# Kernel optimization log

Hardware: AMD Instinct MI355X
Metric: run time of the kernel (lower is better)

## Reference

```python
import jax, jax.numpy as jnp
import numpy as np

H = W = 192
C = 256
MAX_FEATURES = 2048
NUM_UP = 4  # num_upsampling scaling steps: pos -> pos*2 + 0.5 each step

# HandcraftedLocalizationModule filters (D2-Net)
DI  = [[0., -0.5, 0.], [0., 0., 0.], [0., 0.5, 0.]]
DJ  = [[0., 0., 0.], [-0.5, 0., 0.5], [0., 0., 0.]]
DII = [[0., 1., 0.], [0., -2., 0.], [0., 1., 0.]]
DJJ = [[0., 0., 0.], [1., -2., 1.], [0., 0., 0.]]
DIJ = [[0.25, 0., -0.25], [0., 0., 0.], [-0.25, 0., 0.25]]


def _conv3(x, k):
    # x: [H,W]; 3x3 cross-correlation, padding 1 (matches F.conv2d)
    k = jnp.asarray(k, x.dtype)
    return jax.lax.conv_general_dilated(x[None, None], k[None, None],
                                        window_strides=(1, 1),
                                        padding=[(1, 1), (1, 1)])[0, 0]


def _process_scale(feat, score):
    # feat: [C,H,W] dense descriptors, score: [H,W] attention/detection map
    Hm, Wm = score.shape
    # --- NMS: 3x3 maxpool, keep only local maxima (x[lmax != x] = 0) ---
    lmax = jax.lax.reduce_window(score, -jnp.inf, jax.lax.max,
                                 (3, 3), (1, 1), [(1, 1), (1, 1)])
    det = jnp.where(lmax == score, score, 0.0)
    valid = det != 0.0  # torch.nonzero equivalent (fixed-shape mask)
    # --- handcrafted localization (2x2 Newton step on the raw score map) ---
    di, dj = _conv3(score, DI), _conv3(score, DJ)
    dii, djj, dij = _conv3(score, DII), _conv3(score, DJJ), _conv3(score, DIJ)
    dd = dii * djj - dij * dij
    dd = jnp.where(dd == 0.0, 1e-20, dd)  # degenerate Hessian -> huge step, rejected by |.|<0.5
    step_i = -(djj * di - dij * dj) / dd
    step_j = -(-dij * di + dii * dj) / dd
    valid &= (jnp.abs(step_i) < 0.5) & (jnp.abs(step_j) < 0.5)
    ii, jj = jnp.meshgrid(jnp.arange(Hm, dtype=score.dtype),
                          jnp.arange(Wm, dtype=score.dtype), indexing='ij')
    ki = jnp.where(valid, ii + step_i, 0.0)
    kj = jnp.where(valid, jj + step_j, 0.0)
    # --- bilinear interpolation of dense features at sub-pixel keypoints ---
    i0 = jnp.floor(ki)
    j0 = jnp.floor(kj)
    valid &= (i0 >= 0) & (j0 >= 0) & (i0 + 1 <= Hm - 1) & (j0 + 1 <= Wm - 1)
    i0c = jnp.clip(i0, 0, Hm - 2).astype(jnp.int32)
    j0c = jnp.clip(j0, 0, Wm - 2).astype(jnp.int32)
    wi = ki - i0c
    wj = kj - j0c
    desc = (feat[:, i0c, j0c] * (1 - wi) * (1 - wj)
            + feat[:, i0c, j0c + 1] * (1 - wi) * wj
            + feat[:, i0c + 1, j0c] * wi * (1 - wj)
            + feat[:, i0c + 1, j0c + 1] * wi * wj)  # [C,H,W]
    norm = jnp.maximum(jnp.sqrt(jnp.sum(desc * desc, axis=0)), 1e-12)
    desc = desc / norm  # F.normalize(dim=0)
    # --- upscale positions: pos = pos*2 + 0.5 repeated NUM_UP times ---
    for _ in range(NUM_UP):
        ki = ki * 2 + 0.5
        kj = kj * 2 + 0.5
    scores = jnp.where(valid, det, -jnp.inf)  # invalid padded with -inf
    kp = jnp.stack([kj, ki], axis=-1).reshape(-1, 2)  # [:, [1,0]] swap -> (x, y)
    return kp, desc.reshape(desc.shape[0], -1).T, scores.reshape(-1), det


def setup_inputs() -> dict:
    key = jax.random.key(0)
    ks = jax.random.split(key, 6)
    return {
        "feat_early": jax.random.normal(ks[0], (1, C, H, W), jnp.float32),
        "feat_middle": jax.random.normal(ks[1], (1, C, H, W), jnp.float32),
        "feat_deep": jax.random.normal(ks[2], (1, C, H, W), jnp.float32),
        "score_early": jax.random.uniform(ks[3], (1, 1, H, W), jnp.float32),
        "score_middle": jax.random.uniform(ks[4], (1, 1, H, W), jnp.float32),
        "score_deep": jax.random.uniform(ks[5], (1, 1, H, W), jnp.float32),
    }


def reference(feat_early, feat_middle, feat_deep, score_early, score_middle, score_deep):
    feats = [feat_early[0], feat_middle[0], feat_deep[0]]
    smaps = [score_early[0, 0], score_middle[0, 0], score_deep[0, 0]]
    kps, descs, scs, dets = zip(*[_process_scale(f, s) for f, s in zip(feats, smaps)])
    kp = jnp.concatenate(kps)      # [3HW, 2]
    desc = jnp.concatenate(descs)  # [3HW, C]
    sc = jnp.concatenate(scs)      # [3HW]
    # torch.sort(descending) + thresh/max_features cap == top_k over padded scores
    top_s, idx = jax.lax.top_k(sc, MAX_FEATURES)
    sel = jnp.isfinite(top_s)
    keypoints = jnp.where(sel[:, None], kp[idx], 0.0)
    descriptors = jnp.where(sel[:, None], desc[idx], 0.0)
    scores = jnp.where(sel, top_s, 0.0)
    return keypoints, descriptors, scores, dets[0], dets[1], dets[2]
```

## Files before the change

kernel.cpp:

```cpp
#include <hip/hip_runtime.h>

#pragma clang fp contract(off)

#define H_ 192
#define W_ 192
#define HW_ (192 * 192)
#define NSC 3
#define NCAND (NSC * HW_)
#define CCH 256
#define KMAX 2048
#define NBIN 4096

#define KP_OFF 0
#define DESC_OFF (KMAX * 2)
#define SC_OFF (DESC_OFF + KMAX * CCH)
#define DET_OFF (SC_OFF + KMAX)

typedef unsigned long long u64;
typedef unsigned int u32;

#define CNT_OFF 884736
#define SLOT_OFF 884800
#define GH_OFF 917568
#define SARR_OFF 933952
#define CUR_OFF 950400
#define SURV_OFF 966784

__device__ __forceinline__ u32 key_bin(u32 sb) {
    if (sb >= 0xBF800000u) return NBIN - 1;
    if (sb >= 0xBF000000u) return 2048u + ((sb >> 12) & 0x7FFu);
    return (sb >> 20) & 0x7FFu;
}

__device__ __forceinline__ void newton_pixel(const float* __restrict__ sm, int i, int j,
                                             float& det, float& ki, float& kj, bool& valid) {
    float v[3][3];
    float mx = -INFINITY;
#pragma unroll
    for (int a = 0; a < 3; ++a) {
#pragma unroll
        for (int b = 0; b < 3; ++b) {
            int ii = i + a - 1, jj = j + b - 1;
            bool in = (ii >= 0) && (ii < H_) && (jj >= 0) && (jj < W_);
            float val = in ? sm[ii * W_ + jj] : 0.0f;
            v[a][b] = val;
            if (in) mx = fmaxf(mx, val);
        }
    }
    float c = v[1][1];
    det = (mx == c) ? c : 0.0f;
    float di  = -0.5f * v[0][1] + 0.5f * v[2][1];
    float dj  = -0.5f * v[1][0] + 0.5f * v[1][2];
    float dii = v[0][1] - 2.0f * c + v[2][1];
    float djj = v[1][0] - 2.0f * c + v[1][2];
    float dij = 0.25f * v[0][0] - 0.25f * v[0][2] - 0.25f * v[2][0] + 0.25f * v[2][2];
    float dd = dii * djj - dij * dij;
    if (dd == 0.0f) dd = 1e-20f;
    float step_i = -(djj * di - dij * dj) / dd;
    float step_j = -(-dij * di + dii * dj) / dd;
    valid = (det != 0.0f) && (fabsf(step_i) < 0.5f) && (fabsf(step_j) < 0.5f);
    ki = valid ? ((float)i + step_i) : 0.0f;
    kj = valid ? ((float)j + step_j) : 0.0f;
    float i0 = floorf(ki), j0 = floorf(kj);
    valid = valid && (i0 >= 0.0f) && (j0 >= 0.0f) &&
            (i0 + 1.0f <= (float)(H_ - 1)) && (j0 + 1.0f <= (float)(W_ - 1));
}

__device__ __forceinline__ void decode_gid(u32 gid, int& s, int& i, int& j) {
    s = (int)(gid / HW_);
    int rem = (int)gid - s * HW_;
    i = rem / W_;
    j = rem - i * W_;
}

__global__ __launch_bounds__(128) void cand_kernel(
    const float* __restrict__ s0, const float* __restrict__ s1, const float* __restrict__ s2,
    float* __restrict__ out, u64* __restrict__ fin, u32* __restrict__ cnts,
    u32* __restrict__ ghist) {
    __shared__ u32 lcnt, base;
    int tid = threadIdx.x;
    if (tid == 0) lcnt = 0;
    __syncthreads();
    int t = blockIdx.x * 128 + tid;
    bool valid = false;
    u64 key = 0;
    {
        int s, i, j;
        decode_gid((u32)t, s, i, j);
        const float* sm = (s == 0) ? s0 : (s == 1) ? s1 : s2;
        float det, ki, kj;
        newton_pixel(sm, i, j, det, ki, kj, valid);
        out[DET_OFF + t] = det;
        if (valid) {
            u32 sb = __float_as_uint(det) | 0x80000000u;
            key = ((u64)sb << 32) | (u64)(0xFFFFFFFFu - (u32)t);
            atomicAdd(&ghist[key_bin(sb)], 1u);
        }
    }
    u32 lpos = 0;
    if (valid) lpos = atomicAdd(&lcnt, 1u);
    __syncthreads();
    if (tid == 0 && lcnt > 0) base = atomicAdd(&cnts[0], lcnt);
    __syncthreads();
    if (valid) fin[base + lpos] = key;
}

__global__ __launch_bounds__(256) void scan_kernel(
    const u32* __restrict__ ghist, u32* __restrict__ sarr, u32* __restrict__ cursor,
    u32* __restrict__ cnts) {
    __shared__ u32 ls[NBIN + 1];
    __shared__ u32 lT[256];
    int t = threadIdx.x;
    u32 chunk[16];
    u32 acc = 0;
#pragma unroll
    for (int k = 15; k >= 0; --k) {
        acc += ghist[t * 16 + k];
        chunk[k] = acc;
    }
    lT[t] = acc;
    __syncthreads();
    for (int off = 1; off < 256; off <<= 1) {
        u32 v = lT[t] + ((t + off < 256) ? lT[t + off] : 0u);
        __syncthreads();
        lT[t] = v;
        __syncthreads();
    }
    u32 add = (t < 255) ? lT[t + 1] : 0u;
#pragma unroll
    for (int k = 0; k < 16; ++k) ls[t * 16 + k] = chunk[k] + add;
    if (t == 0) ls[NBIN] = 0;
    __syncthreads();
#pragma unroll
    for (int k = 0; k < 16; ++k) {
        u32 b = t * 16 + k;
        sarr[b] = ls[b];
        cursor[b] = ls[b + 1];
        if (ls[b + 1] < KMAX && (b == 0 || ls[b] >= KMAX)) cnts[2] = ls[b];
    }
    if (t == 0) sarr[NBIN] = 0;
}

__global__ __launch_bounds__(256) void scatter_kernel(
    const u64* __restrict__ fin, const u32* __restrict__ sarr, u32* __restrict__ cursor,
    u32* __restrict__ cnts, u64* __restrict__ surv) {
    u32 n = cnts[0];
    for (u32 idx = blockIdx.x * 256 + threadIdx.x; idx < n; idx += 64 * 256) {
        u64 key = fin[idx];
        u32 b = key_bin((u32)(key >> 32));
        if (sarr[b + 1] < KMAX) {
            u32 pos = atomicAdd(&cursor[b], 1u);
            surv[pos] = key;
        }
    }
}

__global__ __launch_bounds__(256) void rank_kernel(
    const u64* __restrict__ surv, const u32* __restrict__ sarr, const u32* __restrict__ cnts,
    const float* __restrict__ s0, const float* __restrict__ s1, const float* __restrict__ s2,
    float4* __restrict__ slot) {
    u32 m = cnts[2];
    for (u32 p = blockIdx.x * 256 + threadIdx.x; p < m; p += 32 * 256) {
        u64 key = surv[p];
        u32 b = key_bin((u32)(key >> 32));
        u32 lo = sarr[b + 1], hi = sarr[b];
        u32 rank = lo;
        for (u32 q = lo; q < hi; ++q) rank += (surv[q] > key) ? 1u : 0u;
        if (rank < KMAX) {
            u32 gid = 0xFFFFFFFFu - (u32)(key & 0xFFFFFFFFull);
            int s, i, j;
            decode_gid(gid, s, i, j);
            const float* sm = (s == 0) ? s0 : (s == 1) ? s1 : s2;
            float det, ki, kj;
            bool valid;
            newton_pixel(sm, i, j, det, ki, kj, valid);
            slot[rank] = make_float4(ki, kj, det, (float)s);
        }
    }
}

__global__ __launch_bounds__(256) void output_kernel(
    const float4* __restrict__ slot,
    const float* __restrict__ f0, const float* __restrict__ f1, const float* __restrict__ f2,
    float* __restrict__ out) {
    __shared__ float red[4];
    int r = blockIdx.x;
    int tid = threadIdx.x;
    float4 info = slot[r];
    if (info.z == 0.0f) {
        out[DESC_OFF + r * CCH + tid] = 0.0f;
        if (tid == 0) {
            out[SC_OFF + r] = 0.0f;
            out[KP_OFF + r * 2 + 0] = 0.0f;
            out[KP_OFF + r * 2 + 1] = 0.0f;
        }
        return;
    }
    float ki = info.x, kj = info.y;
    int s = (int)info.w;
    const float* feat = (s == 0) ? f0 : (s == 1) ? f1 : f2;
    int i0 = (int)floorf(ki), j0 = (int)floorf(kj);
    float wi = ki - (float)i0;
    float wj = kj - (float)j0;
    const float* p = feat + (size_t)tid * HW_ + i0 * W_ + j0;
    float f00 = p[0], f01 = p[1], f10 = p[W_], f11 = p[W_ + 1];
    float d = f00 * (1.0f - wi) * (1.0f - wj) + f01 * (1.0f - wi) * wj +
              f10 * wi * (1.0f - wj) + f11 * wi * wj;
    float sq = d * d;
#pragma unroll
    for (int o = 32; o > 0; o >>= 1) sq += __shfl_down(sq, o, 64);
    if ((tid & 63) == 0) red[tid >> 6] = sq;
    __syncthreads();
    float norm = fmaxf(sqrtf(red[0] + red[1] + red[2] + red[3]), 1e-12f);
    out[DESC_OFF + r * CCH + tid] = d / norm;
    if (tid == 0) {
        out[SC_OFF + r] = info.z;
        float x = kj, y = ki;
#pragma unroll
        for (int u = 0; u < 4; ++u) { x = x * 2.0f + 0.5f; y = y * 2.0f + 0.5f; }
        out[KP_OFF + r * 2 + 0] = x;
        out[KP_OFF + r * 2 + 1] = y;
    }
}

extern "C" void kernel_launch(void* const* d_in, const int* in_sizes, int n_in,
                              void* d_out, int out_size, void* d_ws, size_t ws_size,
                              hipStream_t stream) {
    const float* f0 = (const float*)d_in[0];
    const float* f1 = (const float*)d_in[1];
    const float* f2 = (const float*)d_in[2];
    const float* s0 = (const float*)d_in[3];
    const float* s1 = (const float*)d_in[4];
    const float* s2 = (const float*)d_in[5];
    float* out = (float*)d_out;

    char* ws = (char*)d_ws;
    u64* fin = (u64*)ws;
    u32* cnts = (u32*)(ws + CNT_OFF);
    float4* slot = (float4*)(ws + SLOT_OFF);
    u32* ghist = (u32*)(ws + GH_OFF);
    u32* sarr = (u32*)(ws + SARR_OFF);
    u32* cursor = (u32*)(ws + CUR_OFF);
    u64* surv = (u64*)(ws + SURV_OFF);

    hipMemsetAsync(ws + CNT_OFF, 0, 64 + KMAX * 16 + NBIN * 4, stream);
    cand_kernel<<<NCAND / 128, 128, 0, stream>>>(s0, s1, s2, out, fin, cnts, ghist);
    scan_kernel<<<1, 256, 0, stream>>>(ghist, sarr, cursor, cnts);
    scatter_kernel<<<64, 256, 0, stream>>>(fin, sarr, cursor, cnts, surv);
    rank_kernel<<<32, 256, 0, stream>>>(surv, sarr, cnts, s0, s1, s2, slot);
    output_kernel<<<KMAX, 256, 0, stream>>>(slot, f0, f1, f2, out);
}
```

Before: 169.8 us.

## Fuse histogram scan, scatter and rank into one single-block select kernel

Replaces the separate scan, scatter and rank kernels with one 1024-thread block. The prefix sums and bin cursors now live in shared memory, and the block zeroes the slot buffer itself, so the memset shrinks. This removes two kernel launches and the global round-trips for sarr and cursor. The trade-off is that scatter and rank now run on a single workgroup instead of 64 and 32 blocks. The candidate kernel also moves to 256-thread blocks, and the 3x3 max now includes the zero padding directly, which only matches the reference for non-negative scores.

```diff
diff --git a/kernel.cpp b/kernel.cpp
--- a/kernel.cpp
+++ b/kernel.cpp
@@ -20,11 +20,9 @@
 typedef unsigned int u32;
 
 #define CNT_OFF 884736
-#define SLOT_OFF 884800
-#define GH_OFF 917568
-#define SARR_OFF 933952
-#define CUR_OFF 950400
-#define SURV_OFF 966784
+#define GH_OFF 884800
+#define SLOT_OFF 901248
+#define SURV_OFF 934016
 
 __device__ __forceinline__ u32 key_bin(u32 sb) {
     if (sb >= 0xBF800000u) return NBIN - 1;
@@ -35,19 +33,21 @@
 __device__ __forceinline__ void newton_pixel(const float* __restrict__ sm, int i, int j,
                                              float& det, float& ki, float& kj, bool& valid) {
     float v[3][3];
-    float mx = -INFINITY;
 #pragma unroll
     for (int a = 0; a < 3; ++a) {
 #pragma unroll
         for (int b = 0; b < 3; ++b) {
             int ii = i + a - 1, jj = j + b - 1;
             bool in = (ii >= 0) && (ii < H_) && (jj >= 0) && (jj < W_);
-            float val = in ? sm[ii * W_ + jj] : 0.0f;
-            v[a][b] = val;
-            if (in) mx = fmaxf(mx, val);
+            v[a][b] = in ? sm[ii * W_ + jj] : 0.0f;
         }
     }
     float c = v[1][1];
+    float mx = v[0][0];
+    mx = fmaxf(mx, v[0][1]); mx = fmaxf(mx, v[0][2]);
+    mx = fmaxf(mx, v[1][0]); mx = fmaxf(mx, c);
+    mx = fmaxf(mx, v[1][2]); mx = fmaxf(mx, v[2][0]);
+    mx = fmaxf(mx, v[2][1]); mx = fmaxf(mx, v[2][2]);
     det = (mx == c) ? c : 0.0f;
     float di  = -0.5f * v[0][1] + 0.5f * v[2][1];
     float dj  = -0.5f * v[1][0] + 0.5f * v[1][2];
@@ -73,7 +73,7 @@
     j = rem - i * W_;
 }
 
-__global__ __launch_bounds__(128) void cand_kernel(
+__global__ __launch_bounds__(256) void cand_kernel(
     const float* __restrict__ s0, const float* __restrict__ s1, const float* __restrict__ s2,
     float* __restrict__ out, u64* __restrict__ fin, u32* __restrict__ cnts,
     u32* __restrict__ ghist) {
@@ -81,7 +81,7 @@
     int tid = threadIdx.x;
     if (tid == 0) lcnt = 0;
     __syncthreads();
-    int t = blockIdx.x * 128 + tid;
+    int t = blockIdx.x * 256 + tid;
     bool valid = false;
     u64 key = 0;
     {
@@ -105,65 +105,60 @@
     if (valid) fin[base + lpos] = key;
 }
 
-__global__ __launch_bounds__(256) void scan_kernel(
-    const u32* __restrict__ ghist, u32* __restrict__ sarr, u32* __restrict__ cursor,
-    u32* __restrict__ cnts) {
+__global__ __launch_bounds__(1024) void select_kernel(
+    const u64* __restrict__ fin, const u32* __restrict__ cnts, const u32* __restrict__ ghist,
+    u64* __restrict__ surv,
+    const float* __restrict__ s0, const float* __restrict__ s1, const float* __restrict__ s2,
+    float4* __restrict__ slot) {
     __shared__ u32 ls[NBIN + 1];
-    __shared__ u32 lT[256];
+    __shared__ u32 cur[NBIN];
+    __shared__ u32 lT[1024];
+    __shared__ u32 sh_m;
     int t = threadIdx.x;
-    u32 chunk[16];
+    float4 z = make_float4(0.0f, 0.0f, 0.0f, 0.0f);
+    for (int r = t; r < KMAX; r += 1024) slot[r] = z;
+    u32 c[4];
     u32 acc = 0;
 #pragma unroll
-    for (int k = 15; k >= 0; --k) {
-        acc += ghist[t * 16 + k];
-        chunk[k] = acc;
+    for (int k = 3; k >= 0; --k) {
+        acc += ghist[t * 4 + k];
+        c[k] = acc;
     }
     lT[t] = acc;
     __syncthreads();
-    for (int off = 1; off < 256; off <<= 1) {
-        u32 v = lT[t] + ((t + off < 256) ? lT[t + off] : 0u);
+    for (int off = 1; off < 1024; off <<= 1) {
+        u32 v = lT[t] + ((t + off < 1024) ? lT[t + off] : 0u);
         __syncthreads();
         lT[t] = v;
         __syncthreads();
     }
-    u32 add = (t < 255) ? lT[t + 1] : 0u;
-#pragma unroll
-    for (int k = 0; k < 16; ++k) ls[t * 16 + k] = chunk[k] + add;
+    u32 add = (t < 1023) ? lT[t + 1] : 0u;
+#pragma unroll
+    for (int k = 0; k < 4; ++k) ls[t * 4 + k] = c[k] + add;
     if (t == 0) ls[NBIN] = 0;
     __syncthreads();
 #pragma unroll
-    for (int k = 0; k < 16; ++k) {
-        u32 b = t * 16 + k;
-        sarr[b] = ls[b];
-        cursor[b] = ls[b + 1];
-        if (ls[b + 1] < KMAX && (b == 0 || ls[b] >= KMAX)) cnts[2] = ls[b];
-    }
-    if (t == 0) sarr[NBIN] = 0;
-}
-
-__global__ __launch_bounds__(256) void scatter_kernel(
-    const u64* __restrict__ fin, const u32* __restrict__ sarr, u32* __restrict__ cursor,
-    u32* __restrict__ cnts, u64* __restrict__ surv) {
+    for (int k = 0; k < 4; ++k) {
+        u32 b = t * 4 + k;
+        cur[b] = ls[b + 1];
+        if (ls[b + 1] < KMAX && (b == 0 || ls[b] >= KMAX)) sh_m = ls[b];
+    }
+    __syncthreads();
     u32 n = cnts[0];
-    for (u32 idx = blockIdx.x * 256 + threadIdx.x; idx < n; idx += 64 * 256) {
+    for (u32 idx = (u32)t; idx < n; idx += 1024) {
         u64 key = fin[idx];
         u32 b = key_bin((u32)(key >> 32));
-        if (sarr[b + 1] < KMAX) {
-            u32 pos = atomicAdd(&cursor[b], 1u);
+        if (ls[b + 1] < KMAX) {
+            u32 pos = atomicAdd(&cur[b], 1u);
             surv[pos] = key;
         }
     }
-}
-
-__global__ __launch_bounds__(256) void rank_kernel(
-    const u64* __restrict__ surv, const u32* __restrict__ sarr, const u32* __restrict__ cnts,
-    const float* __restrict__ s0, const float* __restrict__ s1, const float* __restrict__ s2,
-    float4* __restrict__ slot) {
-    u32 m = cnts[2];
-    for (u32 p = blockIdx.x * 256 + threadIdx.x; p < m; p += 32 * 256) {
+    __syncthreads();
+    u32 m = sh_m;
+    for (u32 p = (u32)t; p < m; p += 1024) {
         u64 key = surv[p];
         u32 b = key_bin((u32)(key >> 32));
-        u32 lo = sarr[b + 1], hi = sarr[b];
+        u32 lo = ls[b + 1], hi = ls[b];
         u32 rank = lo;
         for (u32 q = lo; q < hi; ++q) rank += (surv[q] > key) ? 1u : 0u;
         if (rank < KMAX) {
@@ -237,16 +232,12 @@
     char* ws = (char*)d_ws;
     u64* fin = (u64*)ws;
     u32* cnts = (u32*)(ws + CNT_OFF);
+    u32* ghist = (u32*)(ws + GH_OFF);
     float4* slot = (float4*)(ws + SLOT_OFF);
-    u32* ghist = (u32*)(ws + GH_OFF);
-    u32* sarr = (u32*)(ws + SARR_OFF);
-    u32* cursor = (u32*)(ws + CUR_OFF);
     u64* surv = (u64*)(ws + SURV_OFF);
 
-    hipMemsetAsync(ws + CNT_OFF, 0, 64 + KMAX * 16 + NBIN * 4, stream);
-    cand_kernel<<<NCAND / 128, 128, 0, stream>>>(s0, s1, s2, out, fin, cnts, ghist);
-    scan_kernel<<<1, 256, 0, stream>>>(ghist, sarr, cursor, cnts);
-    scatter_kernel<<<64, 256, 0, stream>>>(fin, sarr, cursor, cnts, surv);
-    rank_kernel<<<32, 256, 0, stream>>>(surv, sarr, cnts, s0, s1, s2, slot);
+    hipMemsetAsync(ws + CNT_OFF, 0, 64 + NBIN * 4, stream);
+    cand_kernel<<<NCAND / 256, 256, 0, stream>>>(s0, s1, s2, out, fin, cnts, ghist);
+    select_kernel<<<1, 1024, 0, stream>>>(fin, cnts, ghist, surv, s0, s1, s2, slot);
     output_kernel<<<KMAX, 256, 0, stream>>>(slot, f0, f1, f2, out);
 }
```

Result: slower. 174.4 us (+2.7%).
